# Kernel tuning notes

Measured on AMD Instinct MI355X. Metric: run time of the kernel, lower is better.

## Reference

```python
import jax, jax.numpy as jnp
import numpy as np

N_NODES = 50000
BN_EPS = 1e-5


def setup_inputs() -> dict:
    key = jax.random.key(0)
    ks = jax.random.split(key, 16)
    N, IN, H, OUT, E = N_NODES, 512, 128, 64, 800000
    s = lambda fi, fo: 1.0 / np.sqrt(fi)
    inp = {
        'x': jax.random.normal(ks[0], (N, IN), dtype=jnp.float32),
        'edge_index': jax.random.randint(ks[1], (2, E), 0, N, dtype=jnp.int32),
        # mlpA: Linear(N -> H)
        'WA': jax.random.uniform(ks[2], (H, N), jnp.float32, -s(N, H), s(N, H)),
        'bA': jax.random.uniform(ks[3], (H,), jnp.float32, -s(N, H), s(N, H)),
        # mlpX: Linear(IN -> H)
        'WX': jax.random.uniform(ks[4], (H, IN), jnp.float32, -s(IN, H), s(IN, H)),
        'bX': jax.random.uniform(ks[5], (H,), jnp.float32, -s(IN, H), s(IN, H)),
        # W: Linear(2H -> H)
        'W': jax.random.uniform(ks[6], (H, 2 * H), jnp.float32, -s(2 * H, H), s(2 * H, H)),
        'bW': jax.random.uniform(ks[7], (H,), jnp.float32, -s(2 * H, H), s(2 * H, H)),
        # mlp_final layer 1: Linear(H -> H) + BN
        'Wf1': jax.random.uniform(ks[8], (H, H), jnp.float32, -s(H, H), s(H, H)),
        'bf1': jax.random.uniform(ks[9], (H,), jnp.float32, -s(H, H), s(H, H)),
        'gamma': jnp.ones((H,), jnp.float32),
        'beta': jnp.zeros((H,), jnp.float32),
        # mlp_final layer 2: Linear(H -> OUT)
        'Wf2': jax.random.uniform(ks[10], (OUT, H), jnp.float32, -s(H, OUT), s(H, OUT)),
        'bf2': jax.random.uniform(ks[11], (OUT,), jnp.float32, -s(H, OUT), s(H, OUT)),
    }
    return inp


def _batchnorm(x, gamma, beta):
    # training-mode BN over the node/batch axis (biased variance, as in torch)
    mean = jnp.mean(x, axis=0)
    var = jnp.var(x, axis=0)
    return (x - mean) * jax.lax.rsqrt(var + BN_EPS) * gamma + beta


def reference(x, edge_index, WA, bA, WX, bX, W, bW, Wf1, bf1, gamma, beta, Wf2, bf2):
    row, col = edge_index[0], edge_index[1]
    row = row - row.min()
    # xA = A @ WA.T + bA  where A[i,j]=1 per (row,col) edge (duplicates sum).
    # Equivalent SpMM: gather columns of WA at `col`, segment-sum into `row`.
    xA = jax.ops.segment_sum(WA.T[col], row, num_segments=N_NODES) + bA  # [N, H]
    xX = x @ WX.T + bX  # [N, H]
    h = jnp.concatenate([xA, xX], axis=-1) @ W.T + bW  # [N, H]
    h = jax.nn.relu(h + xA + xX)
    # mlp_final (num_layers=2): Linear -> ReLU -> BN -> (dropout off) -> Linear
    h = jax.nn.relu(h @ Wf1.T + bf1)
    h = _batchnorm(h, gamma, beta)
    out = h @ Wf2.T + bf2  # [N, OUT]
    return out
```

## Files before the change

kernel.cpp:

```cpp
#include <hip/hip_runtime.h>

typedef __bf16 bf16_t;
typedef __bf16 bf16x8 __attribute__((ext_vector_type(8)));
typedef float f32x4 __attribute__((ext_vector_type(4)));

#define IN_DIM 512
#define H_DIM 128
#define OUT_DIM 64
#define BN_EPS 1e-5f
#define SCAN_BLK 2048

#define MFMA(a, b, c) __builtin_amdgcn_mfma_f32_16x16x32_bf16(a, b, c, 0, 0, 0)

__device__ __forceinline__ float ld_adapt(const void* p, size_t i, int isbf) {
    return isbf ? (float)((const bf16_t*)p)[i] : ((const float*)p)[i];
}

__device__ __forceinline__ void split8(const float* p, bf16x8& hi, bf16x8& lo) {
    f32x4 v0 = *(const f32x4*)p;
    f32x4 v1 = *(const f32x4*)(p + 4);
#pragma unroll
    for (int i = 0; i < 8; ++i) {
        float f = (i < 4) ? v0[i] : v1[i - 4];
        bf16_t h = (bf16_t)f;
        hi[i] = h;
        lo[i] = (bf16_t)(f - (float)h);
    }
}

__global__ void k_init(const void* bA, const void* bX, const void* bW, const void* bf1,
                       const void* gamma, const void* beta, const void* bf2,
                       float* __restrict__ dst, int* __restrict__ flag) {
    __shared__ int s_isbf;
    if (threadIdx.x == 0) {
        unsigned u = *(const unsigned*)gamma;
        int f = (u == 0x3F803F80u) ? 1 : 0;
        *flag = f;
        s_isbf = f;
    }
    __syncthreads();
    int isbf = s_isbf;
    int t = threadIdx.x;
    dst[t] = ld_adapt(bA, t, isbf);
    dst[128 + t] = ld_adapt(bX, t, isbf);
    dst[256 + t] = ld_adapt(bW, t, isbf);
    dst[384 + t] = ld_adapt(bf1, t, isbf);
    dst[512 + t] = ld_adapt(gamma, t, isbf);
    dst[640 + t] = ld_adapt(beta, t, isbf);
    if (t < OUT_DIM) dst[768 + t] = ld_adapt(bf2, t, isbf);
}

__global__ __launch_bounds__(256) void k_transpose(const void* __restrict__ WA,
                                                   float* __restrict__ WAT, int N,
                                                   const int* __restrict__ flag) {
    __shared__ float t[64][130];
    int isbf = *flag;
    int n0 = blockIdx.x * 64;
    int tid = threadIdx.x;
#pragma unroll
    for (int i = 0; i < 32; ++i) {
        int lin = i * 256 + tid;
        int h = lin >> 6, nl = lin & 63;
        int n = n0 + nl;
        t[nl][h] = (n < N) ? ld_adapt(WA, (size_t)h * N + n, isbf) : 0.f;
    }
    __syncthreads();
#pragma unroll
    for (int i = 0; i < 32; ++i) {
        int lin = i * 256 + tid;
        int nl = lin >> 7, h = lin & 127;
        int n = n0 + nl;
        if (n < N) WAT[(size_t)n * H_DIM + h] = t[nl][h];
    }
}

__global__ __launch_bounds__(256) void k_prep(const int* __restrict__ rows, int E,
                                              int* __restrict__ bmin, int* __restrict__ cnt) {
    __shared__ int sm[4];
    int i = blockIdx.x * 256 + threadIdx.x;
    int m = 0x7fffffff;
    if (i < E) {
        int r = rows[i];
        m = r;
        atomicAdd(&cnt[r], 1);
    }
    for (int off = 32; off; off >>= 1) m = min(m, __shfl_xor(m, off, 64));
    if ((threadIdx.x & 63) == 0) sm[threadIdx.x >> 6] = m;
    __syncthreads();
    if (threadIdx.x == 0)
        bmin[blockIdx.x] = min(min(sm[0], sm[1]), min(sm[2], sm[3]));
}

__global__ __launch_bounds__(256) void k_scan1(const int* __restrict__ cnt,
                                               int* __restrict__ offs,
                                               int* __restrict__ bsum, int N) {
    __shared__ int ts[256];
    int base = blockIdx.x * SCAN_BLK;
    int t = threadIdx.x;
    int v[8], s = 0;
#pragma unroll
    for (int i = 0; i < 8; ++i) {
        int idx = base + t * 8 + i;
        v[i] = (idx < N) ? cnt[idx] : 0;
        s += v[i];
    }
    ts[t] = s;
    __syncthreads();
    for (int off = 1; off < 256; off <<= 1) {
        int x = (t >= off) ? ts[t - off] : 0;
        __syncthreads();
        ts[t] += x;
        __syncthreads();
    }
    int run = ts[t] - s;
#pragma unroll
    for (int i = 0; i < 8; ++i) {
        int idx = base + t * 8 + i;
        if (idx < N) offs[idx] = run;
        run += v[i];
    }
    if (t == 255) bsum[blockIdx.x] = ts[255];
}

__global__ __launch_bounds__(256) void k_scan2(int* __restrict__ bsum, int* __restrict__ offs,
                                               int NB, int N, const int* __restrict__ bmin,
                                               int nbmin, int* __restrict__ minbuf) {
    __shared__ int sm[256];
    int t = threadIdx.x;
    int m = 0x7fffffff;
    for (int i = t; i < nbmin; i += 256) m = min(m, bmin[i]);
    sm[t] = m;
    __syncthreads();
    for (int off = 128; off; off >>= 1) {
        if (t < off) sm[t] = min(sm[t], sm[t + off]);
        __syncthreads();
    }
    if (t == 0) {
        *minbuf = sm[0];
        int run = 0;
        for (int b = 0; b < NB; ++b) {
            int v = bsum[b];
            bsum[b] = run;
            run += v;
        }
        offs[N] = run;
    }
}

__global__ __launch_bounds__(256) void k_scan3(int* __restrict__ offs, const int* __restrict__ bsum,
                                               int* __restrict__ cursor, int N) {
    int i = blockIdx.x * 256 + threadIdx.x;
    if (i >= N) return;
    int v = offs[i] + bsum[i / SCAN_BLK];
    offs[i] = v;
    cursor[i] = v;
}

__global__ __launch_bounds__(256) void k_build(const int* __restrict__ rows,
                                               const int* __restrict__ cols, int E,
                                               int* __restrict__ cursor,
                                               int* __restrict__ scol) {
    int i = blockIdx.x * 256 + threadIdx.x;
    if (i >= E) return;
    int r = rows[i];
    int pos = atomicAdd(&cursor[r], 1);
    scol[pos] = cols[i];
}

__global__ __launch_bounds__(256) void k_gather(const int* __restrict__ offs,
                                                const int* __restrict__ scol,
                                                const float* __restrict__ WAT,
                                                const float* __restrict__ bA_f,
                                                const int* __restrict__ minbuf,
                                                float* __restrict__ xA, int N) {
    int wave = threadIdx.x >> 6, lane = threadIdx.x & 63;
    int r = blockIdx.x * 4 + wave;
    if (r >= N) return;
    int b = r + *minbuf;
    int s = 0, e = 0;
    if (b < N) {
        s = offs[b];
        e = offs[b + 1];
    }
    float2 a0 = {0.f, 0.f}, a1 = {0.f, 0.f};
    int i = s;
    for (; i + 3 < e; i += 4) {
        int c0 = scol[i], c1 = scol[i + 1], c2 = scol[i + 2], c3 = scol[i + 3];
        float2 w0 = *(const float2*)(WAT + (size_t)c0 * H_DIM + lane * 2);
        float2 w1 = *(const float2*)(WAT + (size_t)c1 * H_DIM + lane * 2);
        float2 w2 = *(const float2*)(WAT + (size_t)c2 * H_DIM + lane * 2);
        float2 w3 = *(const float2*)(WAT + (size_t)c3 * H_DIM + lane * 2);
        a0.x += w0.x + w2.x; a0.y += w0.y + w2.y;
        a1.x += w1.x + w3.x; a1.y += w1.y + w3.y;
    }
    for (; i < e; ++i) {
        int c = scol[i];
        float2 w = *(const float2*)(WAT + (size_t)c * H_DIM + lane * 2);
        a0.x += w.x; a0.y += w.y;
    }
    float2 bias = *(const float2*)(bA_f + lane * 2);
    float2 out = {a0.x + a1.x + bias.x, a0.y + a1.y + bias.y};
    *(float2*)(xA + (size_t)r * H_DIM + lane * 2) = out;
}

__device__ __forceinline__ void pack_frag(const void* __restrict__ W, bf16_t* __restrict__ hi,
                                          bf16_t* __restrict__ lo, int K, int NC,
                                          int addres, int isbf, int f, int lane) {
    int ks = f / (NC >> 4), nt = f % (NC >> 4);
    int n = nt * 16 + (lane & 15);
    int k0 = ks * 32 + (lane >> 4) * 8;
    bf16_t* dh = hi + (size_t)f * 512 + lane * 8;
    bf16_t* dl = lo + (size_t)f * 512 + lane * 8;
#pragma unroll
    for (int j = 0; j < 8; ++j) {
        int kk = k0 + j;
        float v = ld_adapt(W, (size_t)n * K + kk, isbf);
        if (addres && (kk == n || kk == n + H_DIM)) v += 1.f;
        bf16_t h = (bf16_t)v;
        dh[j] = h;
        dl[j] = (bf16_t)(v - (float)h);
    }
}

__global__ __launch_bounds__(256) void k_pack3(const void* WX, bf16_t* WXh, bf16_t* WXl,
                                               const void* W, bf16_t* Wh, bf16_t* Wl,
                                               const void* Wf1, bf16_t* Wf1h, bf16_t* Wf1l,
                                               const int* __restrict__ flag) {
    int g = blockIdx.x * 256 + threadIdx.x;
    int f = g >> 6, lane = g & 63;
    int isbf = *flag;
    if (f < 128)
        pack_frag(WX, WXh, WXl, IN_DIM, H_DIM, 0, isbf, f, lane);
    else if (f < 192)
        pack_frag(W, Wh, Wl, 2 * H_DIM, H_DIM, 1, isbf, f - 128, lane);
    else if (f < 224)
        pack_frag(Wf1, Wf1h, Wf1l, H_DIM, H_DIM, 0, isbf, f - 192, lane);
}

__global__ __launch_bounds__(256) void k_fuseA(
    const void* __restrict__ x, const float* __restrict__ xAf,
    const bf16_t* __restrict__ WXh, const bf16_t* __restrict__ WXl,
    const bf16_t* __restrict__ Wh, const bf16_t* __restrict__ Wl,
    const bf16_t* __restrict__ Wf1h, const bf16_t* __restrict__ Wf1l,
    const float* __restrict__ smallf, float* __restrict__ h2,
    double* __restrict__ sums, double* __restrict__ sumsq,
    const int* __restrict__ flag, int M) {
    __shared__ float axx[4][16 * 132];
    __shared__ float ls_sum[H_DIM], ls_sq[H_DIM];
    int tid = threadIdx.x;
    int wave = tid >> 6, lane = tid & 63, l16 = lane & 15, quad = lane >> 4;
    int mbase = blockIdx.x * 64 + wave * 16;
    int isbf = *flag;
    float* ax = axx[wave];
    int r0 = min(mbase + l16, M - 1);
    const float* bX = smallf + 128;
    const float* bW = smallf + 256;
    const float* bf1 = smallf + 384;

    if (tid < H_DIM) {
        ls_sum[tid] = 0.f;
        ls_sq[tid] = 0.f;
    }
    __syncthreads();

    bf16x8 zero8;
#pragma unroll
    for (int i = 0; i < 8; ++i) zero8[i] = (bf16_t)0.f;

    f32x4 acc[8];
#pragma unroll
    for (int nt = 0; nt < 8; ++nt) acc[nt] = f32x4{0.f, 0.f, 0.f, 0.f};
    {
        size_t offx = (size_t)r0 * IN_DIM + quad * 8;
        for (int ks = 0; ks < 16; ++ks) {
            bf16x8 ah, al;
            if (isbf) {
                ah = *(const bf16x8*)((const bf16_t*)x + offx + ks * 32);
                al = zero8;
            } else {
                split8((const float*)x + offx + ks * 32, ah, al);
            }
            const bf16_t* bhp = WXh + (size_t)ks * 8 * 512 + lane * 8;
            const bf16_t* blp = WXl + (size_t)ks * 8 * 512 + lane * 8;
#pragma unroll
            for (int nt = 0; nt < 8; ++nt) {
                bf16x8 bh = *(const bf16x8*)(bhp + nt * 512);
                bf16x8 bl = *(const bf16x8*)(blp + nt * 512);
                acc[nt] = MFMA(ah, bh, acc[nt]);
                acc[nt] = MFMA(ah, bl, acc[nt]);
                acc[nt] = MFMA(al, bh, acc[nt]);
            }
        }
    }
#pragma unroll
    for (int nt = 0; nt < 8; ++nt) {
        int col = nt * 16 + l16;
        float b = bX[col];
#pragma unroll
        for (int r = 0; r < 4; ++r) {
            int lr = quad * 4 + r;
            ax[lr * 132 + col] = acc[nt][r] + b;
        }
    }

#pragma unroll
    for (int nt = 0; nt < 8; ++nt) acc[nt] = f32x4{0.f, 0.f, 0.f, 0.f};
    for (int ks = 0; ks < 8; ++ks) {
        bf16x8 ah, al;
        if (ks < 4)
            split8(xAf + (size_t)r0 * H_DIM + ks * 32 + quad * 8, ah, al);
        else
            split8(ax + l16 * 132 + (ks - 4) * 32 + quad * 8, ah, al);
        const bf16_t* bhp = Wh + (size_t)ks * 8 * 512 + lane * 8;
        const bf16_t* blp = Wl + (size_t)ks * 8 * 512 + lane * 8;
#pragma unroll
        for (int nt = 0; nt < 8; ++nt) {
            bf16x8 bh = *(const bf16x8*)(bhp + nt * 512);
            bf16x8 bl = *(const bf16x8*)(blp + nt * 512);
            acc[nt] = MFMA(ah, bh, acc[nt]);
            acc[nt] = MFMA(ah, bl, acc[nt]);
            acc[nt] = MFMA(al, bh, acc[nt]);
        }
    }
#pragma unroll
    for (int nt = 0; nt < 8; ++nt) {
        int col = nt * 16 + l16;
        float b = bW[col];
#pragma unroll
        for (int r = 0; r < 4; ++r) {
            int lr = quad * 4 + r;
            ax[lr * 132 + col] = fmaxf(acc[nt][r] + b, 0.f);
        }
    }

#pragma unroll
    for (int nt = 0; nt < 8; ++nt) acc[nt] = f32x4{0.f, 0.f, 0.f, 0.f};
    for (int ks = 0; ks < 4; ++ks) {
        bf16x8 ah, al;
        split8(ax + l16 * 132 + ks * 32 + quad * 8, ah, al);
        const bf16_t* bhp = Wf1h + (size_t)ks * 8 * 512 + lane * 8;
        const bf16_t* blp = Wf1l + (size_t)ks * 8 * 512 + lane * 8;
#pragma unroll
        for (int nt = 0; nt < 8; ++nt) {
            bf16x8 bh = *(const bf16x8*)(bhp + nt * 512);
            bf16x8 bl = *(const bf16x8*)(blp + nt * 512);
            acc[nt] = MFMA(ah, bh, acc[nt]);
            acc[nt] = MFMA(ah, bl, acc[nt]);
            acc[nt] = MFMA(al, bh, acc[nt]);
        }
    }
#pragma unroll
    for (int nt = 0; nt < 8; ++nt) {
        int col = nt * 16 + l16;
        float b = bf1[col];
        float s = 0.f, s2 = 0.f;
#pragma unroll
        for (int r = 0; r < 4; ++r) {
            int row = mbase + quad * 4 + r;
            if (row < M) {
                float v = fmaxf(acc[nt][r] + b, 0.f);
                h2[(size_t)row * H_DIM + col] = v;
                s += v;
                s2 += v * v;
            }
        }
        s += __shfl_xor(s, 16, 64);
        s += __shfl_xor(s, 32, 64);
        s2 += __shfl_xor(s2, 16, 64);
        s2 += __shfl_xor(s2, 32, 64);
        if (quad == 0) {
            atomicAdd(&ls_sum[col], s);
            atomicAdd(&ls_sq[col], s2);
        }
    }
    __syncthreads();
    if (tid < H_DIM) {
        atomicAdd(&sums[tid], (double)ls_sum[tid]);
        atomicAdd(&sumsq[tid], (double)ls_sq[tid]);
    }
}

__global__ __launch_bounds__(256) void k_fuseB(
    const float* __restrict__ h2, const void* __restrict__ Wf2,
    const float* __restrict__ smallf, const double* __restrict__ sums,
    const double* __restrict__ sumsq, void* __restrict__ outv,
    const int* __restrict__ flag, int M) {
    __shared__ bf16_t wh[16 * 512];
    __shared__ bf16_t wl[16 * 512];
    __shared__ float aw[H_DIM], cw[H_DIM], b2[OUT_DIM];
    int t = threadIdx.x;
    int isbf = *flag;
    const float* gamma_f = smallf + 512;
    const float* beta_f = smallf + 640;
    const float* bf2_f = smallf + 768;

    if (t < H_DIM) {
        double mean = sums[t] / (double)M;
        double var = sumsq[t] / (double)M - mean * mean;
        if (var < 0) var = 0;
        float a = gamma_f[t] * rsqrtf((float)var + BN_EPS);
        aw[t] = a;
        cw[t] = beta_f[t] - (float)mean * a;
    }
    __syncthreads();
    if (t < OUT_DIM) {
        float acc = bf2_f[t];
        for (int j = 0; j < H_DIM; ++j) acc += ld_adapt(Wf2, (size_t)t * H_DIM + j, isbf) * cw[j];
        b2[t] = acc;
    }
    for (int u = t; u < 1024; u += 256) {
        int f = u >> 6, ln = u & 63;
        int ks = f >> 2, nt = f & 3;
        int n = nt * 16 + (ln & 15);
        int k0 = ks * 32 + (ln >> 4) * 8;
#pragma unroll
        for (int j = 0; j < 8; ++j) {
            float v = ld_adapt(Wf2, (size_t)n * H_DIM + k0 + j, isbf) * aw[k0 + j];
            bf16_t h = (bf16_t)v;
            wh[f * 512 + ln * 8 + j] = h;
            wl[f * 512 + ln * 8 + j] = (bf16_t)(v - (float)h);
        }
    }
    __syncthreads();

    int wave = t >> 6, lane = t & 63, l16 = lane & 15, quad = lane >> 4;
    int mbase = blockIdx.x * 64 + wave * 16;
    int r0 = min(mbase + l16, M - 1);
    f32x4 acc4[4];
#pragma unroll
    for (int nt = 0; nt < 4; ++nt) acc4[nt] = f32x4{0.f, 0.f, 0.f, 0.f};
    for (int ks = 0; ks < 4; ++ks) {
        bf16x8 ah, al;
        split8(h2 + (size_t)r0 * H_DIM + ks * 32 + quad * 8, ah, al);
#pragma unroll
        for (int nt = 0; nt < 4; ++nt) {
            bf16x8 bh = *(const bf16x8*)(wh + (ks * 4 + nt) * 512 + lane * 8);
            bf16x8 bl = *(const bf16x8*)(wl + (ks * 4 + nt) * 512 + lane * 8);
            acc4[nt] = MFMA(ah, bh, acc4[nt]);
            acc4[nt] = MFMA(ah, bl, acc4[nt]);
            acc4[nt] = MFMA(al, bh, acc4[nt]);
        }
    }
#pragma unroll
    for (int nt = 0; nt < 4; ++nt) {
        int col = nt * 16 + l16;
        float b = b2[col];
#pragma unroll
        for (int r = 0; r < 4; ++r) {
            int row = mbase + quad * 4 + r;
            if (row < M) {
                float v = acc4[nt][r] + b;
                if (isbf)
                    ((bf16_t*)outv)[(size_t)row * OUT_DIM + col] = (bf16_t)v;
                else
                    ((float*)outv)[(size_t)row * OUT_DIM + col] = v;
            }
        }
    }
}

extern "C" void kernel_launch(void* const* d_in, const int* in_sizes, int n_in,
                              void* d_out, int out_size, void* d_ws, size_t ws_size,
                              hipStream_t stream) {
    const void* x = d_in[0];
    const int* ei = (const int*)d_in[1];
    const void* WA = d_in[2];
    const void* bA = d_in[3];
    const void* WX = d_in[4];
    const void* bX = d_in[5];
    const void* W = d_in[6];
    const void* bW = d_in[7];
    const void* Wf1 = d_in[8];
    const void* bf1 = d_in[9];
    const void* gamma = d_in[10];
    const void* beta = d_in[11];
    const void* Wf2 = d_in[12];
    const void* bf2 = d_in[13];

    const int N = in_sizes[0] / IN_DIM;
    const int E = in_sizes[1] / 2;
    const int* rows = ei;
    const int* cols = ei + E;
    const int eblocks = (E + 255) / 256;

    char* ws = (char*)d_ws;
    size_t off = 0;
    auto alloc = [&](size_t bytes) {
        char* p = ws + off;
        off += (bytes + 255) & ~(size_t)255;
        return p;
    };
    int* flag = (int*)alloc(4);
    int* minbuf = (int*)alloc(4);
    float* smallf = (float*)alloc(832 * 4);
    double* sums = (double*)alloc(2 * H_DIM * 8);
    double* sumsq = sums + H_DIM;
    bf16_t* WXp_h = (bf16_t*)alloc((size_t)IN_DIM * H_DIM * 2);
    bf16_t* WXp_l = (bf16_t*)alloc((size_t)IN_DIM * H_DIM * 2);
    bf16_t* Wp_h = (bf16_t*)alloc((size_t)256 * H_DIM * 2);
    bf16_t* Wp_l = (bf16_t*)alloc((size_t)256 * H_DIM * 2);
    bf16_t* Wf1p_h = (bf16_t*)alloc((size_t)H_DIM * H_DIM * 2);
    bf16_t* Wf1p_l = (bf16_t*)alloc((size_t)H_DIM * H_DIM * 2);
    int* cnt = (int*)alloc((size_t)N * 4);
    int* offs = (int*)alloc(((size_t)N + 1) * 4);
    int* cursor = (int*)alloc((size_t)N * 4);
    int* bsum = (int*)alloc(64 * 4);
    int* bmin = (int*)alloc((size_t)eblocks * 4);
    int* scol = (int*)alloc((size_t)E * 4);
    float* WAT = (float*)alloc((size_t)N * H_DIM * 4);
    float* xAf = (float*)alloc((size_t)N * H_DIM * 4);
    float* h2 = WAT;

    float* bA_f = smallf + 0;

    hipMemsetAsync(cnt, 0, (size_t)N * 4, stream);
    hipMemsetAsync(sums, 0, 2 * H_DIM * 8, stream);

    k_init<<<1, 128, 0, stream>>>(bA, bX, bW, bf1, gamma, beta, bf2, smallf, flag);
    k_transpose<<<(N + 63) / 64, 256, 0, stream>>>(WA, WAT, N, flag);
    k_pack3<<<56, 256, 0, stream>>>(WX, WXp_h, WXp_l, W, Wp_h, Wp_l, Wf1, Wf1p_h, Wf1p_l, flag);

    k_prep<<<eblocks, 256, 0, stream>>>(rows, E, bmin, cnt);
    int NB = (N + SCAN_BLK - 1) / SCAN_BLK;
    k_scan1<<<NB, 256, 0, stream>>>(cnt, offs, bsum, N);
    k_scan2<<<1, 256, 0, stream>>>(bsum, offs, NB, N, bmin, eblocks, minbuf);
    k_scan3<<<(N + 255) / 256, 256, 0, stream>>>(offs, bsum, cursor, N);
    k_build<<<eblocks, 256, 0, stream>>>(rows, cols, E, cursor, scol);
    k_gather<<<(N + 3) / 4, 256, 0, stream>>>(offs, scol, WAT, bA_f, minbuf, xAf, N);

    int fblocks = (N + 63) / 64;
    k_fuseA<<<fblocks, 256, 0, stream>>>(x, xAf, WXp_h, WXp_l, Wp_h, Wp_l, Wf1p_h, Wf1p_l,
                                         smallf, h2, sums, sumsq, flag, N);
    k_fuseB<<<fblocks, 256, 0, stream>>>(h2, Wf2, smallf, sums, sumsq, d_out, flag, N);
}
```

Measured before the change: 484.8 us.

## Split fused MLP N-dimension across two wave halves with shared LDS tile

k_fuseA now launches 512 threads per block, and each 16-row band is handled by two waves that each compute half of the 128 output columns (4 n-tiles instead of 8). The per-wave LDS scratch becomes one shared 64x132 tile, and __syncthreads barriers are added between stages so each wave can read columns written by its partner wave. This halves accumulator registers per wave and doubles the number of waves, aiming for more latency hiding. The cost is extra barriers, and both waves now load the x row fragments and redo the bf16 splitting, so A-operand traffic doubles.

```diff
diff --git a/kernel.cpp b/kernel.cpp
--- a/kernel.cpp
+++ b/kernel.cpp
@@ -237,7 +237,7 @@
         pack_frag(Wf1, Wf1h, Wf1l, H_DIM, H_DIM, 0, isbf, f - 192, lane);
 }
 
-__global__ __launch_bounds__(256) void k_fuseA(
+__global__ __launch_bounds__(512) void k_fuseA(
     const void* __restrict__ x, const float* __restrict__ xAf,
     const bf16_t* __restrict__ WXh, const bf16_t* __restrict__ WXl,
     const bf16_t* __restrict__ Wh, const bf16_t* __restrict__ Wl,
@@ -245,13 +245,14 @@
     const float* __restrict__ smallf, float* __restrict__ h2,
     double* __restrict__ sums, double* __restrict__ sumsq,
     const int* __restrict__ flag, int M) {
-    __shared__ float axx[4][16 * 132];
+    __shared__ float ax[64 * 132];
     __shared__ float ls_sum[H_DIM], ls_sq[H_DIM];
     int tid = threadIdx.x;
     int wave = tid >> 6, lane = tid & 63, l16 = lane & 15, quad = lane >> 4;
-    int mbase = blockIdx.x * 64 + wave * 16;
+    int band = wave & 3, half = wave >> 2;
+    int ntb = half * 4;
+    int mbase = blockIdx.x * 64 + band * 16;
     int isbf = *flag;
-    float* ax = axx[wave];
     int r0 = min(mbase + l16, M - 1);
     const float* bX = smallf + 128;
     const float* bW = smallf + 256;
@@ -261,15 +262,14 @@
         ls_sum[tid] = 0.f;
         ls_sq[tid] = 0.f;
     }
-    __syncthreads();
 
     bf16x8 zero8;
 #pragma unroll
     for (int i = 0; i < 8; ++i) zero8[i] = (bf16_t)0.f;
 
-    f32x4 acc[8];
-#pragma unroll
-    for (int nt = 0; nt < 8; ++nt) acc[nt] = f32x4{0.f, 0.f, 0.f, 0.f};
+    f32x4 acc[4];
+#pragma unroll
+    for (int nt = 0; nt < 4; ++nt) acc[nt] = f32x4{0.f, 0.f, 0.f, 0.f};
     {
         size_t offx = (size_t)r0 * IN_DIM + quad * 8;
         for (int ks = 0; ks < 16; ++ks) {
@@ -280,10 +280,10 @@
             } else {
                 split8((const float*)x + offx + ks * 32, ah, al);
             }
-            const bf16_t* bhp = WXh + (size_t)ks * 8 * 512 + lane * 8;
-            const bf16_t* blp = WXl + (size_t)ks * 8 * 512 + lane * 8;
-#pragma unroll
-            for (int nt = 0; nt < 8; ++nt) {
+            const bf16_t* bhp = WXh + ((size_t)ks * 8 + ntb) * 512 + lane * 8;
+            const bf16_t* blp = WXl + ((size_t)ks * 8 + ntb) * 512 + lane * 8;
+#pragma unroll
+            for (int nt = 0; nt < 4; ++nt) {
                 bf16x8 bh = *(const bf16x8*)(bhp + nt * 512);
                 bf16x8 bl = *(const bf16x8*)(blp + nt * 512);
                 acc[nt] = MFMA(ah, bh, acc[nt]);
@@ -293,28 +293,29 @@
         }
     }
 #pragma unroll
-    for (int nt = 0; nt < 8; ++nt) {
-        int col = nt * 16 + l16;
+    for (int nt = 0; nt < 4; ++nt) {
+        int col = (ntb + nt) * 16 + l16;
         float b = bX[col];
 #pragma unroll
         for (int r = 0; r < 4; ++r) {
-            int lr = quad * 4 + r;
+            int lr = band * 16 + quad * 4 + r;
             ax[lr * 132 + col] = acc[nt][r] + b;
         }
     }
-
-#pragma unroll
-    for (int nt = 0; nt < 8; ++nt) acc[nt] = f32x4{0.f, 0.f, 0.f, 0.f};
+    __syncthreads();
+
+#pragma unroll
+    for (int nt = 0; nt < 4; ++nt) acc[nt] = f32x4{0.f, 0.f, 0.f, 0.f};
     for (int ks = 0; ks < 8; ++ks) {
         bf16x8 ah, al;
         if (ks < 4)
             split8(xAf + (size_t)r0 * H_DIM + ks * 32 + quad * 8, ah, al);
         else
-            split8(ax + l16 * 132 + (ks - 4) * 32 + quad * 8, ah, al);
-        const bf16_t* bhp = Wh + (size_t)ks * 8 * 512 + lane * 8;
-        const bf16_t* blp = Wl + (size_t)ks * 8 * 512 + lane * 8;
-#pragma unroll
-        for (int nt = 0; nt < 8; ++nt) {
+            split8(ax + (band * 16 + l16) * 132 + (ks - 4) * 32 + quad * 8, ah, al);
+        const bf16_t* bhp = Wh + ((size_t)ks * 8 + ntb) * 512 + lane * 8;
+        const bf16_t* blp = Wl + ((size_t)ks * 8 + ntb) * 512 + lane * 8;
+#pragma unroll
+        for (int nt = 0; nt < 4; ++nt) {
             bf16x8 bh = *(const bf16x8*)(bhp + nt * 512);
             bf16x8 bl = *(const bf16x8*)(blp + nt * 512);
             acc[nt] = MFMA(ah, bh, acc[nt]);
@@ -322,26 +323,28 @@
             acc[nt] = MFMA(al, bh, acc[nt]);
         }
     }
-#pragma unroll
-    for (int nt = 0; nt < 8; ++nt) {
-        int col = nt * 16 + l16;
+    __syncthreads();
+#pragma unroll
+    for (int nt = 0; nt < 4; ++nt) {
+        int col = (ntb + nt) * 16 + l16;
         float b = bW[col];
 #pragma unroll
         for (int r = 0; r < 4; ++r) {
-            int lr = quad * 4 + r;
+            int lr = band * 16 + quad * 4 + r;
             ax[lr * 132 + col] = fmaxf(acc[nt][r] + b, 0.f);
         }
     }
-
-#pragma unroll
-    for (int nt = 0; nt < 8; ++nt) acc[nt] = f32x4{0.f, 0.f, 0.f, 0.f};
+    __syncthreads();
+
+#pragma unroll
+    for (int nt = 0; nt < 4; ++nt) acc[nt] = f32x4{0.f, 0.f, 0.f, 0.f};
     for (int ks = 0; ks < 4; ++ks) {
         bf16x8 ah, al;
-        split8(ax + l16 * 132 + ks * 32 + quad * 8, ah, al);
-        const bf16_t* bhp = Wf1h + (size_t)ks * 8 * 512 + lane * 8;
-        const bf16_t* blp = Wf1l + (size_t)ks * 8 * 512 + lane * 8;
-#pragma unroll
-        for (int nt = 0; nt < 8; ++nt) {
+        split8(ax + (band * 16 + l16) * 132 + ks * 32 + quad * 8, ah, al);
+        const bf16_t* bhp = Wf1h + ((size_t)ks * 8 + ntb) * 512 + lane * 8;
+        const bf16_t* blp = Wf1l + ((size_t)ks * 8 + ntb) * 512 + lane * 8;
+#pragma unroll
+        for (int nt = 0; nt < 4; ++nt) {
             bf16x8 bh = *(const bf16x8*)(bhp + nt * 512);
             bf16x8 bl = *(const bf16x8*)(blp + nt * 512);
             acc[nt] = MFMA(ah, bh, acc[nt]);
@@ -350,8 +353,8 @@
         }
     }
 #pragma unroll
-    for (int nt = 0; nt < 8; ++nt) {
-        int col = nt * 16 + l16;
+    for (int nt = 0; nt < 4; ++nt) {
+        int col = (ntb + nt) * 16 + l16;
         float b = bf1[col];
         float s = 0.f, s2 = 0.f;
 #pragma unroll
@@ -529,7 +532,7 @@
     k_gather<<<(N + 3) / 4, 256, 0, stream>>>(offs, scol, WAT, bA_f, minbuf, xAf, N);
 
     int fblocks = (N + 63) / 64;
-    k_fuseA<<<fblocks, 256, 0, stream>>>(x, xAf, WXp_h, WXp_l, Wp_h, Wp_l, Wf1p_h, Wf1p_l,
+    k_fuseA<<<fblocks, 512, 0, stream>>>(x, xAf, WXp_h, WXp_l, Wp_h, Wp_l, Wf1p_h, Wf1p_l,
                                          smallf, h2, sums, sumsq, flag, N);
     k_fuseB<<<fblocks, 256, 0, stream>>>(h2, Wf2, smallf, sums, sumsq, d_out, flag, N);
 }
```

Result: no change. 487.7 us (+0.6%).
